# Optimization experiments

Hardware: AMD Instinct MI355X
Metric: run time of the kernel (lower is better)

The kernel has to match this reference:

```python
import jax, jax.numpy as jnp
import numpy as np
from jax import lax

B, T, C = 32, 512, 128
K = 3                      # top_k periods
MIN_P, MAX_P = 8, 64       # period search band
P_MAX = MAX_P              # grid width
CYC_MAX = (T + MIN_P - 1) // MIN_P
KW = 9                     # cyc-axis depthwise kernel
GN_G = 32                  # _best_gn_groups(128)
EPS_GN = 1e-5
EPS_ORTH = 1e-6
EPS_W = 1e-8


def setup_inputs() -> dict:
    key = jax.random.key(0)
    ks = jax.random.split(key, 4)
    return {
        "x": jax.random.normal(ks[0], (B, T, C), jnp.float32),
        "W_dw": jax.random.normal(ks[1], (C, 1, KW), jnp.float32) * 0.1,
        "W_pw": jax.random.normal(ks[2], (C, C), jnp.float32) * (1.0 / np.sqrt(C)),
        "gn_weight": jnp.ones((C,), jnp.float32),
        "gn_bias": jnp.zeros((C,), jnp.float32),
        "W_gate": jax.random.normal(ks[3], (C, C), jnp.float32) * (1.0 / np.sqrt(C)),
        "gamma": jnp.full((C,), 1e-3, jnp.float32),
    }


def _autocorr_topk(x):
    # x: [B,T,C] -> period idx [B,K], softmax weights [B,K]
    Xf = jnp.fft.rfft(x, axis=1)
    Pm = (Xf * jnp.conj(Xf)).real.mean(-1)          # [B, T//2+1]
    r = jnp.fft.irfft(Pm, n=T, axis=1)              # [B, T] autocorrelation
    lag = jnp.arange(T)
    valid = (lag >= MIN_P) & (lag <= MAX_P)
    very_neg = jnp.finfo(x.dtype).min / 8
    rm = jnp.where(valid[None, :], r, very_neg)
    vals, idx = lax.top_k(rm, K)
    w = jax.nn.softmax(vals, axis=1)
    return idx, w


def _fold(s, p):
    # s: [N,T,C], p: [N] int periods -> Z [N,C,CYC_MAX,P_MAX], mask, unfold index maps
    N = s.shape[0]
    p = jnp.maximum(p, 1)
    tpad = ((T + p - 1) // p) * p                   # [N]
    cyc = jnp.arange(CYC_MAX)[None, :, None]
    pos = jnp.arange(P_MAX)[None, None, :]
    time = cyc * p[:, None, None] + pos             # [N,CYC_MAX,P_MAX]
    valid = (pos < p[:, None, None]) & (time < tpad[:, None, None])
    # right-side reflect padding indices
    m = 2 * (T - 1)
    rr = time % m
    src_idx = jnp.where(rr < T, rr, m - rr)
    src = jnp.take_along_axis(s, src_idx.reshape(N, -1)[:, :, None], axis=1)
    src = src.reshape(N, CYC_MAX, P_MAX, C) * valid[..., None].astype(s.dtype)
    Z = jnp.transpose(src, (0, 3, 1, 2))            # [N,C,CYC_MAX,P_MAX]
    mask2d = valid[:, None].astype(s.dtype)         # [N,1,CYC_MAX,P_MAX]
    t = jnp.arange(T)[None, :]
    cyc_T = jnp.clip(t // p[:, None], 0, CYC_MAX - 1)
    pos_T = jnp.clip(t % p[:, None], 0, P_MAX - 1)
    return Z, mask2d, cyc_T, pos_T


def _cyc_conv(Z, mask2d, W_dw, W_pw, gn_w, gn_b, W_gate, gamma):
    # CycAxisConv1d: mean over period axis, depthwise+pointwise conv along cyc,
    # GroupNorm, GELU, SE-gate, LayerScale residual broadcast back to 2D.
    N, _, L, _ = Z.shape
    u = Z.mean(-1)                                  # [N,C,L]
    h = lax.conv_general_dilated(u, W_dw, (1,), [(KW // 2, KW // 2)],
                                 dimension_numbers=('NCH', 'OIH', 'NCH'),
                                 feature_group_count=C)
    h = jnp.einsum('oc,ncl->nol', W_pw, h)
    hg = h.reshape(N, GN_G, C // GN_G, L)
    mean = hg.mean((2, 3), keepdims=True)
    var = hg.var((2, 3), keepdims=True)
    hg = (hg - mean) * lax.rsqrt(var + EPS_GN)
    h = hg.reshape(N, C, L) * gn_w[None, :, None] + gn_b[None, :, None]
    h = jax.nn.gelu(h, approximate=False)
    gate = jax.nn.sigmoid(jnp.einsum('oc,nc->no', W_gate, u.mean(-1)))
    h = h * gate[:, :, None]
    x2d = h[..., None] * gamma[None, :, None, None] * mask2d
    return Z + x2d


def _unfold(Z, cyc_T, pos_T):
    N = Z.shape[0]
    Zf = Z.reshape(N, C, CYC_MAX * P_MAX)
    sp = jnp.clip(cyc_T * P_MAX + pos_T, 0, CYC_MAX * P_MAX - 1)  # [N,T]
    y = jnp.take_along_axis(Zf, sp[:, None, :], axis=2)           # [N,C,T]
    return jnp.transpose(y, (0, 2, 1))                            # [N,T,C]


def reference(x, W_dw, W_pw, gn_weight, gn_bias, W_gate, gamma):
    idx, w = _autocorr_topk(x)                      # [B,K], [B,K]
    p_flat = idx.reshape(-1)                        # [B*K]
    s = jnp.repeat(x, K, axis=0)                    # [B*K,T,C]
    Z, mask2d, cyc_T, pos_T = _fold(s, p_flat)
    Z = _cyc_conv(Z, mask2d, W_dw, W_pw, gn_weight, gn_bias, W_gate, gamma)
    y = _unfold(Z, cyc_T, pos_T).reshape(B, K, T, C)
    periodic = jnp.einsum('bk,bktc->btc', w, y)
    # period confidence Gamma from weight entropy
    H = -(w * jnp.log(w + EPS_W)).sum(1)
    Gamma = jnp.clip(1.0 - H / (jnp.log(float(K) + EPS_W) + EPS_W), 0.0, 1.0)
    # orthogonal residual of local part against periodic part
    local = x - periodic
    num = (local * periodic).sum(1, keepdims=True)
    den = (periodic * periodic).sum(1, keepdims=True) + EPS_ORTH
    local_orth = local - num / den * periodic
    g = Gamma[:, None, None]
    return g * (periodic + local_orth) + (1.0 - g) * x
```

## Files before the change

### kernel.cpp

```cpp
#include <hip/hip_runtime.h>
#include <math.h>

static constexpr int Bn   = 32;
static constexpr int Tn   = 512;
static constexpr int Cn   = 128;
static constexpr int NLAG = 57;
static constexpr int CYC  = 64;

__device__ __forceinline__ int topk_p(const float* __restrict__ rb,
                                      int tid, int kk) {
  float v  = (tid < NLAG) ? rb[tid] : -INFINITY;
  int  idx = tid;
  int  lag = 8;
#pragma unroll
  for (int k = 0; k < 3; ++k) {
    if (k > kk) break;
    float bv = v; int bi = idx;
#pragma unroll
    for (int m = 32; m > 0; m >>= 1) {
      const float ov = __shfl_xor(bv, m, 64);
      const int   oi = __shfl_xor(bi, m, 64);
      if (ov > bv || (ov == bv && oi < bi)) { bv = ov; bi = oi; }
    }
    lag = bi + 8;
    if (idx == bi) v = -INFINITY;
  }
  return lag;
}

__global__ __launch_bounds__(256) void k_autocorr(const float* __restrict__ x,
    float* __restrict__ r_ws) {
  const int w   = (blockIdx.x & 7) * 32 + (blockIdx.x >> 3);
  const int b   = w >> 3;
  const int grp = w & 7;
  const int L0  = 8 + grp * 8;
  const int tid = threadIdx.x;
  const float4* X4 = (const float4*)(x + (size_t)b * Tn * Cn);

  float acc[8];
#pragma unroll
  for (int i = 0; i < 8; ++i) acc[i] = 0.f;

  for (int it = 0; it < 8; ++it) {
    const int id = it * 256 + tid;
    const int c4 = id & 31;
    const int t0 = (id >> 5) * 8;
    float4 A[8];
#pragma unroll
    for (int j = 0; j < 8; ++j) A[j] = X4[(t0 + j) * 32 + c4];
    float4 R[16];
#pragma unroll
    for (int j = 0; j < 16; ++j) R[j] = X4[((t0 + L0 + j) & 511) * 32 + c4];
#pragma unroll
    for (int g = 0; g < 8; ++g) {
#pragma unroll
      for (int j = 0; j < 8; ++j) {
        const float4 a = A[j];
        const float4 r = R[g + j];
        acc[g] += a.x * r.x + a.y * r.y + a.z * r.z + a.w * r.w;
      }
    }
  }

  __shared__ float lds_r[4][8];
  const int lane = tid & 63, wave = tid >> 6;
#pragma unroll
  for (int g = 0; g < 8; ++g) {
    float v = acc[g];
#pragma unroll
    for (int m = 32; m > 0; m >>= 1) v += __shfl_xor(v, m, 64);
    if (lane == 0) lds_r[wave][g] = v;
  }
  __syncthreads();
  if (tid < 8) {
    const int li = grp * 8 + tid;
    if (li < NLAG) {
      r_ws[b * NLAG + li] =
          (lds_r[0][tid] + lds_r[1][tid] + lds_r[2][tid] + lds_r[3][tid]) * (1.0f / Cn);
    }
  }
}

__global__ __launch_bounds__(128) void k_fold_u(const float* __restrict__ x,
    const float* __restrict__ r_ws, float* __restrict__ u) {
  const int bid = blockIdx.x;
  const int w = (bid & 7) * 768 + (bid >> 3);
  const int n = w >> 6, l = w & 63;
  const int b = n / 3, kk = n % 3;
  const int tid = threadIdx.x;

  __shared__ int p_sh;
  if (tid < 64) {
    const int lag = topk_p(r_ws + b * NLAG, tid, kk);
    if (tid == 0) p_sh = lag;
  }
  __syncthreads();
  const int p    = p_sh;
  const int ncyc = (Tn + p - 1) / p;

  float acc = 0.f;
  if (l < ncyc) {
    const float* xb = x + (size_t)b * Tn * Cn;
    const int base = l * p;
    for (int j = 0; j < p; ++j) {
      const int time = base + j;
      const int src  = time < Tn ? time : (2 * (Tn - 1) - time);
      acc += xb[src * Cn + tid];
    }
  }
  u[((size_t)n * CYC + l) * Cn + tid] = acc * (1.0f / 64.0f);
}

__global__ __launch_bounds__(256) void k_conv(
    const float* __restrict__ u, const float* __restrict__ Wdw,
    const float* __restrict__ Wpw, const float* __restrict__ gnw,
    const float* __restrict__ gnb, const float* __restrict__ Wgate,
    float* __restrict__ hh) {
  const int bid = blockIdx.x;
  const int w = (bid & 7) * 96 + (bid >> 3);
  const int n = w >> 3, og = w & 7;
  const int tid  = threadIdx.x;
  const int l    = tid & 63;
  const int wq   = __builtin_amdgcn_readfirstlane(tid >> 6);

  __shared__ float smem[8320];
  __shared__ float ubar_s[Cn];

  {
    const float4* u4 = (const float4*)(u + (size_t)n * CYC * Cn);
#pragma unroll
    for (int i = 0; i < 8; ++i) {
      const int idx4 = i * 256 + tid;
      const float4 v = u4[idx4];
      const int ll = idx4 >> 5;
      const int cc = (idx4 & 31) << 2;
      float* d = smem + ll * 129 + cc;
      d[0] = v.x; d[1] = v.y; d[2] = v.z; d[3] = v.w;
    }
  }
  __syncthreads();

  if (tid < Cn) {
    float s = 0.f;
    for (int ll = 0; ll < CYC; ++ll) s += smem[ll * 129 + tid];
    ubar_s[tid] = s * (1.0f / CYC);
  }

  float hreg[32];
  {
    const int c0 = wq * 32;
#pragma unroll
    for (int i = 0; i < 32; ++i) {
      const int c = c0 + i;
      float s = 0.f;
#pragma unroll
      for (int k = 0; k < 9; ++k) {
        const int ll = l + k - 4;
        if (ll >= 0 && ll < CYC) s += smem[ll * 129 + c] * Wdw[c * 9 + k];
      }
      hreg[i] = s;
    }
  }
  __syncthreads();

  float gi[4];
  {
    const int ol   = l & 3;
    const int part = l >> 2;
    const int o    = og * 16 + wq * 4 + ol;
    float z = 0.f;
    const float* wg = Wgate + (size_t)o * Cn + part * 8;
    const float* ub = ubar_s + part * 8;
#pragma unroll
    for (int cc = 0; cc < 8; ++cc) z += wg[cc] * ub[cc];
    z += __shfl_xor(z, 4, 64);
    z += __shfl_xor(z, 8, 64);
    z += __shfl_xor(z, 16, 64);
    z += __shfl_xor(z, 32, 64);
    const float sig = 1.0f / (1.0f + expf(-z));
#pragma unroll
    for (int i = 0; i < 4; ++i) gi[i] = __shfl(sig, i, 64);
  }

  {
    const int c0 = wq * 32;
#pragma unroll
    for (int i = 0; i < 32; ++i) smem[(c0 + i) * 65 + l] = hreg[i];
  }
  __syncthreads();

  const int o4 = og * 16 + wq * 4;
  float acc[4];
#pragma unroll
  for (int i = 0; i < 4; ++i) acc[i] = 0.f;
  const float* wb = Wpw + (size_t)o4 * Cn;
  for (int c = 0; c < Cn; ++c) {
    const float hv = smem[c * 65 + l];
#pragma unroll
    for (int i = 0; i < 4; ++i) acc[i] = fmaf(wb[i * Cn + c], hv, acc[i]);
  }

  float s1 = acc[0] + acc[1] + acc[2] + acc[3];
  float s2 = acc[0]*acc[0] + acc[1]*acc[1] + acc[2]*acc[2] + acc[3]*acc[3];
#pragma unroll
  for (int m = 32; m > 0; m >>= 1) {
    s1 += __shfl_xor(s1, m, 64);
    s2 += __shfl_xor(s2, m, 64);
  }
  const float mean = s1 * (1.0f / 256.0f);
  const float var  = s2 * (1.0f / 256.0f) - mean * mean;
  const float rstd = rsqrtf(var + 1e-5f);

  float4 res;
  float* rp = (float*)&res;
#pragma unroll
  for (int i = 0; i < 4; ++i) {
    const int o = o4 + i;
    float h = (acc[i] - mean) * rstd;
    h = h * gnw[o] + gnb[o];
    h = 0.5f * h * (1.0f + erff(h * 0.70710678118654752440f));
    rp[i] = h * gi[i];
  }
  *(float4*)(hh + (size_t)n * CYC * Cn + (size_t)l * Cn + o4) = res;
}

__global__ __launch_bounds__(256) void k_dot_out(
    const float* __restrict__ x, const float* __restrict__ hh,
    const float* __restrict__ r_ws, const float* __restrict__ gamma,
    float* __restrict__ out) {
  const int bid = blockIdx.x;
  const int w = (bid & 7) * 32 + (bid >> 3);
  const int b = w >> 3, cg = w & 7;
  const int tid = threadIdx.x;
  const int c_l = tid & 15;
  const int tg  = tid >> 4;
  const int c   = cg * 16 + c_l;

  __shared__ float P_s[Tn * 16];
  __shared__ unsigned short cyc_s[Tn][3];
  __shared__ float params[4];
  __shared__ int   pp[3];
  __shared__ float red[2][4][16];
  __shared__ float sc_s[16];

  if (tid < 64) {
    const float* rb = r_ws + b * NLAG;
    float v  = (tid < NLAG) ? rb[tid] : -INFINITY;
    int  idx = tid;
    float vals[3]; int lags[3];
#pragma unroll
    for (int k = 0; k < 3; ++k) {
      float bv = v; int bi = idx;
#pragma unroll
      for (int m = 32; m > 0; m >>= 1) {
        const float ov = __shfl_xor(bv, m, 64);
        const int   oi = __shfl_xor(bi, m, 64);
        if (ov > bv || (ov == bv && oi < bi)) { bv = ov; bi = oi; }
      }
      vals[k] = bv; lags[k] = bi + 8;
      if (idx == bi) v = -INFINITY;
    }
    if (tid == 0) {
      const float m  = vals[0];
      const float e0 = expf(vals[0] - m), e1 = expf(vals[1] - m), e2 = expf(vals[2] - m);
      const float s  = e0 + e1 + e2;
      const float w0 = e0 / s, w1 = e1 / s, w2 = e2 / s;
      pp[0] = lags[0]; pp[1] = lags[1]; pp[2] = lags[2];
      params[0] = w0; params[1] = w1; params[2] = w2;
      const float H  = -(w0 * logf(w0 + 1e-8f) + w1 * logf(w1 + 1e-8f) + w2 * logf(w2 + 1e-8f));
      const float lg = logf(3.0f + 1e-8f) + 1e-8f;
      params[3] = fminf(fmaxf(1.0f - H / lg, 0.0f), 1.0f);
    }
  }
  __syncthreads();
  const int p0 = pp[0], p1 = pp[1], p2 = pp[2];
  const float w0 = params[0], w1 = params[1], w2 = params[2];
  const float g  = params[3];
  const float sw = w0 + w1 + w2;

  for (int t = tid; t < Tn; t += 256) {
    cyc_s[t][0] = (unsigned short)(t / p0);
    cyc_s[t][1] = (unsigned short)(t / p1);
    cyc_s[t][2] = (unsigned short)(t / p2);
  }
  __syncthreads();

  const float gam = gamma[c];
  const float* xb = x + (size_t)b * Tn * Cn;
  const float* h0 = hh + (size_t)(b * 3 + 0) * CYC * Cn + c;
  const float* h1 = hh + (size_t)(b * 3 + 1) * CYC * Cn + c;
  const float* h2 = hh + (size_t)(b * 3 + 2) * CYC * Cn + c;

  float na = 0.f, da = 0.f;
#pragma unroll 4
  for (int tt = 0; tt < 32; ++tt) {
    const int t = tt * 16 + tg;
    const float xv = xb[t * Cn + c];
    const float dv = gam * (w0 * h0[cyc_s[t][0] * Cn] +
                            w1 * h1[cyc_s[t][1] * Cn] +
                            w2 * h2[cyc_s[t][2] * Cn]);
    const float P = sw * xv + dv;
    P_s[t * 16 + c_l] = P;
    na += (xv - P) * P;
    da += P * P;
  }
  na += __shfl_xor(na, 16, 64); da += __shfl_xor(da, 16, 64);
  na += __shfl_xor(na, 32, 64); da += __shfl_xor(da, 32, 64);
  const int wv_ = tid >> 6;
  if ((tid & 63) < 16) { red[0][wv_][c_l] = na; red[1][wv_][c_l] = da; }
  __syncthreads();
  if (tid < 16) {
    const float num = red[0][0][tid] + red[0][1][tid] + red[0][2][tid] + red[0][3][tid];
    const float den = red[1][0][tid] + red[1][1][tid] + red[1][2][tid] + red[1][3][tid] + 1e-6f;
    sc_s[tid] = g * (num / den);
  }
  __syncthreads();
  const float sc = sc_s[c_l];

  float* ob = out + (size_t)b * Tn * Cn;
#pragma unroll 4
  for (int tt = 0; tt < 32; ++tt) {
    const int t = tt * 16 + tg;
    const float xv = xb[t * Cn + c];
    ob[t * Cn + c] = xv - sc * P_s[t * 16 + c_l];
  }
}

extern "C" void kernel_launch(void* const* d_in, const int* in_sizes, int n_in,
                              void* d_out, int out_size, void* d_ws, size_t ws_size,
                              hipStream_t stream) {
  const float* x     = (const float*)d_in[0];
  const float* Wdw   = (const float*)d_in[1];
  const float* Wpw   = (const float*)d_in[2];
  const float* gnw   = (const float*)d_in[3];
  const float* gnb   = (const float*)d_in[4];
  const float* Wgate = (const float*)d_in[5];
  const float* gamma = (const float*)d_in[6];
  float* out = (float*)d_out;

  char* ws = (char*)d_ws;
  float* r_ws = (float*)ws;
  float* u    = (float*)(ws + 8192);
  float* hh   = (float*)(ws + 8192 + 3145728);

  k_autocorr<<<Bn * 8, 256, 0, stream>>>(x, r_ws);
  k_fold_u<<<6144, 128, 0, stream>>>(x, r_ws, u);
  k_conv<<<768, 256, 0, stream>>>(u, Wdw, Wpw, gnw, gnb, Wgate, hh);
  k_dot_out<<<256, 256, 0, stream>>>(x, hh, r_ws, gamma, out);
}
```

Measured before the change: 138.9 us.

## Fuse four kernels into one cooperative persistent kernel with grid syncs

Replaces the four-kernel chain (autocorr, fold, conv, output) with a single cooperative kernel of 512 blocks that runs each stage in turn, separated by grid.sync(). Work is remapped per stage: autocorr uses 16 groups of 4 lags per batch, fold runs 12 units per block, and conv runs 1 or 2 units per block. The aim is to remove kernel launch gaps and tail effects between stages. In exchange it adds grid-wide barrier cost and uneven work per block in the conv and output stages. If the cooperative launch fails, it falls back to the old four launches.

```diff
diff --git a/kernel.cpp b/kernel.cpp
--- a/kernel.cpp
+++ b/kernel.cpp
@@ -1,5 +1,8 @@
 #include <hip/hip_runtime.h>
+#include <hip/hip_cooperative_groups.h>
 #include <math.h>
+
+namespace cg = cooperative_groups;
 
 static constexpr int Bn   = 32;
 static constexpr int Tn   = 512;
@@ -8,9 +11,9 @@
 static constexpr int CYC  = 64;
 
 __device__ __forceinline__ int topk_p(const float* __restrict__ rb,
-                                      int tid, int kk) {
-  float v  = (tid < NLAG) ? rb[tid] : -INFINITY;
-  int  idx = tid;
+                                      int lane, int kk) {
+  float v  = (lane < NLAG) ? rb[lane] : -INFINITY;
+  int  idx = lane;
   int  lag = 8;
 #pragma unroll
   for (int k = 0; k < 3; ++k) {
@@ -26,6 +29,320 @@
     if (idx == bi) v = -INFINITY;
   }
   return lag;
+}
+
+__device__ __forceinline__ void conv_unit(
+    int n, int og, int tid,
+    const float* __restrict__ u, const float* __restrict__ Wdw,
+    const float* __restrict__ Wpw, const float* __restrict__ gnw,
+    const float* __restrict__ gnb, const float* __restrict__ Wgate,
+    float* __restrict__ hh, float* smem, float* ubar_s) {
+  const int l  = tid & 63;
+  const int wq = __builtin_amdgcn_readfirstlane(tid >> 6);
+
+  __syncthreads();
+
+  {
+    const float4* u4 = (const float4*)(u + (size_t)n * CYC * Cn);
+#pragma unroll
+    for (int i = 0; i < 8; ++i) {
+      const int idx4 = i * 256 + tid;
+      const float4 v = u4[idx4];
+      const int ll = idx4 >> 5;
+      const int cc = (idx4 & 31) << 2;
+      float* d = smem + ll * 129 + cc;
+      d[0] = v.x; d[1] = v.y; d[2] = v.z; d[3] = v.w;
+    }
+  }
+  __syncthreads();
+
+  if (tid < Cn) {
+    float s = 0.f;
+    for (int ll = 0; ll < CYC; ++ll) s += smem[ll * 129 + tid];
+    ubar_s[tid] = s * (1.0f / CYC);
+  }
+
+  float hreg[32];
+  {
+    const int c0 = wq * 32;
+#pragma unroll
+    for (int i = 0; i < 32; ++i) {
+      const int c = c0 + i;
+      float s = 0.f;
+#pragma unroll
+      for (int k = 0; k < 9; ++k) {
+        const int ll = l + k - 4;
+        if (ll >= 0 && ll < CYC) s += smem[ll * 129 + c] * Wdw[c * 9 + k];
+      }
+      hreg[i] = s;
+    }
+  }
+  __syncthreads();
+
+  float gi[4];
+  {
+    const int ol   = l & 3;
+    const int part = l >> 2;
+    const int o    = og * 16 + wq * 4 + ol;
+    float z = 0.f;
+    const float* wg = Wgate + (size_t)o * Cn + part * 8;
+    const float* ub = ubar_s + part * 8;
+#pragma unroll
+    for (int cc = 0; cc < 8; ++cc) z += wg[cc] * ub[cc];
+    z += __shfl_xor(z, 4, 64);
+    z += __shfl_xor(z, 8, 64);
+    z += __shfl_xor(z, 16, 64);
+    z += __shfl_xor(z, 32, 64);
+    const float sig = 1.0f / (1.0f + expf(-z));
+#pragma unroll
+    for (int i = 0; i < 4; ++i) gi[i] = __shfl(sig, i, 64);
+  }
+
+  {
+    const int c0 = wq * 32;
+#pragma unroll
+    for (int i = 0; i < 32; ++i) smem[(c0 + i) * 65 + l] = hreg[i];
+  }
+  __syncthreads();
+
+  const int o4 = og * 16 + wq * 4;
+  float acc[4];
+#pragma unroll
+  for (int i = 0; i < 4; ++i) acc[i] = 0.f;
+  const float* wb = Wpw + (size_t)o4 * Cn;
+  for (int c = 0; c < Cn; ++c) {
+    const float hv = smem[c * 65 + l];
+#pragma unroll
+    for (int i = 0; i < 4; ++i) acc[i] = fmaf(wb[i * Cn + c], hv, acc[i]);
+  }
+
+  float s1 = acc[0] + acc[1] + acc[2] + acc[3];
+  float s2 = acc[0]*acc[0] + acc[1]*acc[1] + acc[2]*acc[2] + acc[3]*acc[3];
+#pragma unroll
+  for (int m = 32; m > 0; m >>= 1) {
+    s1 += __shfl_xor(s1, m, 64);
+    s2 += __shfl_xor(s2, m, 64);
+  }
+  const float mean = s1 * (1.0f / 256.0f);
+  const float var  = s2 * (1.0f / 256.0f) - mean * mean;
+  const float rstd = rsqrtf(var + 1e-5f);
+
+  float4 res;
+  float* rp = (float*)&res;
+#pragma unroll
+  for (int i = 0; i < 4; ++i) {
+    const int o = o4 + i;
+    float h = (acc[i] - mean) * rstd;
+    h = h * gnw[o] + gnb[o];
+    h = 0.5f * h * (1.0f + erff(h * 0.70710678118654752440f));
+    rp[i] = h * gi[i];
+  }
+  *(float4*)(hh + (size_t)n * CYC * Cn + (size_t)l * Cn + o4) = res;
+}
+
+__global__ __launch_bounds__(256, 2) void mega(
+    const float* __restrict__ x, const float* __restrict__ Wdw,
+    const float* __restrict__ Wpw, const float* __restrict__ gnw,
+    const float* __restrict__ gnb, const float* __restrict__ Wgate,
+    const float* __restrict__ gamma, float* __restrict__ r_ws,
+    float* __restrict__ u, float* __restrict__ hh, float* __restrict__ out) {
+  cg::grid_group grid = cg::this_grid();
+  const int bid = blockIdx.x;
+  const int ws  = (bid & 7) * 64 + (bid >> 3);
+  const int xcd = ws >> 6;
+  const int tid = threadIdx.x;
+
+  __shared__ float smem[8320];
+  __shared__ float ubar_s[Cn];
+  __shared__ unsigned short cyc_s[Tn][3];
+  __shared__ float ldsr[4][4];
+  __shared__ int   pslot[12];
+  __shared__ float red_s[2][4][16];
+  __shared__ float sc_s[16];
+  __shared__ float par_s[4];
+  __shared__ int   pp_s[3];
+
+  {
+    const int b   = ws >> 4;
+    const int grp = ws & 15;
+    const int L0  = 8 + grp * 4;
+    const float4* X4 = (const float4*)(x + (size_t)b * Tn * Cn);
+
+    float acc[4];
+#pragma unroll
+    for (int i = 0; i < 4; ++i) acc[i] = 0.f;
+
+    for (int it = 0; it < 8; ++it) {
+      const int id = it * 256 + tid;
+      const int c4 = id & 31;
+      const int t0 = (id >> 5) * 8;
+      float4 A[8];
+#pragma unroll
+      for (int j = 0; j < 8; ++j) A[j] = X4[(t0 + j) * 32 + c4];
+      float4 R[11];
+#pragma unroll
+      for (int j = 0; j < 11; ++j) R[j] = X4[((t0 + L0 + j) & 511) * 32 + c4];
+#pragma unroll
+      for (int g = 0; g < 4; ++g) {
+#pragma unroll
+        for (int j = 0; j < 8; ++j) {
+          const float4 a = A[j];
+          const float4 r = R[g + j];
+          acc[g] += a.x * r.x + a.y * r.y + a.z * r.z + a.w * r.w;
+        }
+      }
+    }
+
+    const int lane = tid & 63, wv = tid >> 6;
+#pragma unroll
+    for (int g = 0; g < 4; ++g) {
+      float v = acc[g];
+#pragma unroll
+      for (int m = 32; m > 0; m >>= 1) v += __shfl_xor(v, m, 64);
+      if (lane == 0) ldsr[wv][g] = v;
+    }
+    __syncthreads();
+    if (tid < 4) {
+      const int li = grp * 4 + tid;
+      if (li < NLAG) {
+        r_ws[b * NLAG + li] =
+            (ldsr[0][tid] + ldsr[1][tid] + ldsr[2][tid] + ldsr[3][tid]) * (1.0f / Cn);
+      }
+    }
+  }
+  grid.sync();
+
+  {
+    for (int it2 = 0; it2 < 6; ++it2) {
+      const int sub  = tid >> 7;
+      const int unit = ws * 12 + it2 * 2 + sub;
+      const int n = unit >> 6, l = unit & 63;
+      const int b = n / 3, kk = n % 3;
+      if ((tid & 64) == 0) {
+        const int lag = topk_p(r_ws + b * NLAG, tid & 63, kk);
+        if ((tid & 63) == 0) pslot[it2 * 2 + sub] = lag;
+      }
+      __syncthreads();
+      const int p    = pslot[it2 * 2 + sub];
+      const int ncyc = (Tn + p - 1) / p;
+      const int c    = tid & 127;
+      float acc = 0.f;
+      if (l < ncyc) {
+        const float* xb = x + (size_t)b * Tn * Cn;
+        const int base = l * p;
+        for (int j = 0; j < p; ++j) {
+          const int time = base + j;
+          const int src  = time < Tn ? time : (2 * (Tn - 1) - time);
+          acc += xb[src * Cn + c];
+        }
+      }
+      u[((size_t)n * CYC + l) * Cn + c] = acc * (1.0f / 64.0f);
+    }
+  }
+  grid.sync();
+
+  {
+    const int j0 = ws & 63;
+    conv_unit(12 * xcd + (j0 >> 3), j0 & 7, tid,
+              u, Wdw, Wpw, gnw, gnb, Wgate, hh, smem, ubar_s);
+    if (bid < 256) {
+      const int j1 = 64 + (ws & 31);
+      conv_unit(12 * xcd + (j1 >> 3), j1 & 7, tid,
+                u, Wdw, Wpw, gnw, gnb, Wgate, hh, smem, ubar_s);
+    }
+  }
+  grid.sync();
+
+  if (bid < 256) {
+    const int unit = xcd * 32 + (ws & 31);
+    const int b = unit >> 3, cgp = unit & 7;
+    const int c_l = tid & 15;
+    const int tg  = tid >> 4;
+    const int c   = cgp * 16 + c_l;
+    float* P_s = smem;
+
+    if (tid < 64) {
+      const float* rb = r_ws + b * NLAG;
+      float v  = (tid < NLAG) ? rb[tid] : -INFINITY;
+      int  idx = tid;
+      float vals[3]; int lags[3];
+#pragma unroll
+      for (int k = 0; k < 3; ++k) {
+        float bv = v; int bi = idx;
+#pragma unroll
+        for (int m = 32; m > 0; m >>= 1) {
+          const float ov = __shfl_xor(bv, m, 64);
+          const int   oi = __shfl_xor(bi, m, 64);
+          if (ov > bv || (ov == bv && oi < bi)) { bv = ov; bi = oi; }
+        }
+        vals[k] = bv; lags[k] = bi + 8;
+        if (idx == bi) v = -INFINITY;
+      }
+      if (tid == 0) {
+        const float m  = vals[0];
+        const float e0 = expf(vals[0] - m), e1 = expf(vals[1] - m), e2 = expf(vals[2] - m);
+        const float s  = e0 + e1 + e2;
+        const float w0 = e0 / s, w1 = e1 / s, w2 = e2 / s;
+        pp_s[0] = lags[0]; pp_s[1] = lags[1]; pp_s[2] = lags[2];
+        par_s[0] = w0; par_s[1] = w1; par_s[2] = w2;
+        const float H  = -(w0 * logf(w0 + 1e-8f) + w1 * logf(w1 + 1e-8f) + w2 * logf(w2 + 1e-8f));
+        const float lg = logf(3.0f + 1e-8f) + 1e-8f;
+        par_s[3] = fminf(fmaxf(1.0f - H / lg, 0.0f), 1.0f);
+      }
+    }
+    __syncthreads();
+    const int p0 = pp_s[0], p1 = pp_s[1], p2 = pp_s[2];
+    const float w0 = par_s[0], w1 = par_s[1], w2 = par_s[2];
+    const float g  = par_s[3];
+    const float sw = w0 + w1 + w2;
+
+    for (int t = tid; t < Tn; t += 256) {
+      cyc_s[t][0] = (unsigned short)(t / p0);
+      cyc_s[t][1] = (unsigned short)(t / p1);
+      cyc_s[t][2] = (unsigned short)(t / p2);
+    }
+    __syncthreads();
+
+    const float gam = gamma[c];
+    const float* xb = x + (size_t)b * Tn * Cn;
+    const float* h0 = hh + (size_t)(b * 3 + 0) * CYC * Cn + c;
+    const float* h1 = hh + (size_t)(b * 3 + 1) * CYC * Cn + c;
+    const float* h2 = hh + (size_t)(b * 3 + 2) * CYC * Cn + c;
+
+    float na = 0.f, da = 0.f;
+#pragma unroll 4
+    for (int tt = 0; tt < 32; ++tt) {
+      const int t = tt * 16 + tg;
+      const float xv = xb[t * Cn + c];
+      const float dv = gam * (w0 * h0[cyc_s[t][0] * Cn] +
+                              w1 * h1[cyc_s[t][1] * Cn] +
+                              w2 * h2[cyc_s[t][2] * Cn]);
+      const float P = sw * xv + dv;
+      P_s[t * 16 + c_l] = P;
+      na += (xv - P) * P;
+      da += P * P;
+    }
+    na += __shfl_xor(na, 16, 64); da += __shfl_xor(da, 16, 64);
+    na += __shfl_xor(na, 32, 64); da += __shfl_xor(da, 32, 64);
+    const int wv_ = tid >> 6;
+    if ((tid & 63) < 16) { red_s[0][wv_][c_l] = na; red_s[1][wv_][c_l] = da; }
+    __syncthreads();
+    if (tid < 16) {
+      const float num = red_s[0][0][tid] + red_s[0][1][tid] + red_s[0][2][tid] + red_s[0][3][tid];
+      const float den = red_s[1][0][tid] + red_s[1][1][tid] + red_s[1][2][tid] + red_s[1][3][tid] + 1e-6f;
+      sc_s[tid] = g * (num / den);
+    }
+    __syncthreads();
+    const float sc = sc_s[c_l];
+
+    float* ob = out + (size_t)b * Tn * Cn;
+#pragma unroll 4
+    for (int tt = 0; tt < 32; ++tt) {
+      const int t = tt * 16 + tg;
+      const float xv = xb[t * Cn + c];
+      ob[t * Cn + c] = xv - sc * P_s[t * 16 + c_l];
+    }
+  }
 }
 
 __global__ __launch_bounds__(256) void k_autocorr(const float* __restrict__ x,
@@ -40,7 +357,6 @@
   float acc[8];
 #pragma unroll
   for (int i = 0; i < 8; ++i) acc[i] = 0.f;
-
   for (int it = 0; it < 8; ++it) {
     const int id = it * 256 + tid;
     const int c4 = id & 31;
@@ -61,7 +377,6 @@
       }
     }
   }
-
   __shared__ float lds_r[4][8];
   const int lane = tid & 63, wave = tid >> 6;
 #pragma unroll
@@ -74,10 +389,9 @@
   __syncthreads();
   if (tid < 8) {
     const int li = grp * 8 + tid;
-    if (li < NLAG) {
+    if (li < NLAG)
       r_ws[b * NLAG + li] =
           (lds_r[0][tid] + lds_r[1][tid] + lds_r[2][tid] + lds_r[3][tid]) * (1.0f / Cn);
-    }
   }
 }
 
@@ -88,16 +402,14 @@
   const int n = w >> 6, l = w & 63;
   const int b = n / 3, kk = n % 3;
   const int tid = threadIdx.x;
-
   __shared__ int p_sh;
   if (tid < 64) {
     const int lag = topk_p(r_ws + b * NLAG, tid, kk);
     if (tid == 0) p_sh = lag;
   }
   __syncthreads();
-  const int p    = p_sh;
+  const int p = p_sh;
   const int ncyc = (Tn + p - 1) / p;
-
   float acc = 0.f;
   if (l < ncyc) {
     const float* xb = x + (size_t)b * Tn * Cn;
@@ -119,109 +431,9 @@
   const int bid = blockIdx.x;
   const int w = (bid & 7) * 96 + (bid >> 3);
   const int n = w >> 3, og = w & 7;
-  const int tid  = threadIdx.x;
-  const int l    = tid & 63;
-  const int wq   = __builtin_amdgcn_readfirstlane(tid >> 6);
-
   __shared__ float smem[8320];
   __shared__ float ubar_s[Cn];
-
-  {
-    const float4* u4 = (const float4*)(u + (size_t)n * CYC * Cn);
-#pragma unroll
-    for (int i = 0; i < 8; ++i) {
-      const int idx4 = i * 256 + tid;
-      const float4 v = u4[idx4];
-      const int ll = idx4 >> 5;
-      const int cc = (idx4 & 31) << 2;
-      float* d = smem + ll * 129 + cc;
-      d[0] = v.x; d[1] = v.y; d[2] = v.z; d[3] = v.w;
-    }
-  }
-  __syncthreads();
-
-  if (tid < Cn) {
-    float s = 0.f;
-    for (int ll = 0; ll < CYC; ++ll) s += smem[ll * 129 + tid];
-    ubar_s[tid] = s * (1.0f / CYC);
-  }
-
-  float hreg[32];
-  {
-    const int c0 = wq * 32;
-#pragma unroll
-    for (int i = 0; i < 32; ++i) {
-      const int c = c0 + i;
-      float s = 0.f;
-#pragma unroll
-      for (int k = 0; k < 9; ++k) {
-        const int ll = l + k - 4;
-        if (ll >= 0 && ll < CYC) s += smem[ll * 129 + c] * Wdw[c * 9 + k];
-      }
-      hreg[i] = s;
-    }
-  }
-  __syncthreads();
-
-  float gi[4];
-  {
-    const int ol   = l & 3;
-    const int part = l >> 2;
-    const int o    = og * 16 + wq * 4 + ol;
-    float z = 0.f;
-    const float* wg = Wgate + (size_t)o * Cn + part * 8;
-    const float* ub = ubar_s + part * 8;
-#pragma unroll
-    for (int cc = 0; cc < 8; ++cc) z += wg[cc] * ub[cc];
-    z += __shfl_xor(z, 4, 64);
-    z += __shfl_xor(z, 8, 64);
-    z += __shfl_xor(z, 16, 64);
-    z += __shfl_xor(z, 32, 64);
-    const float sig = 1.0f / (1.0f + expf(-z));
-#pragma unroll
-    for (int i = 0; i < 4; ++i) gi[i] = __shfl(sig, i, 64);
-  }
-
-  {
-    const int c0 = wq * 32;
-#pragma unroll
-    for (int i = 0; i < 32; ++i) smem[(c0 + i) * 65 + l] = hreg[i];
-  }
-  __syncthreads();
-
-  const int o4 = og * 16 + wq * 4;
-  float acc[4];
-#pragma unroll
-  for (int i = 0; i < 4; ++i) acc[i] = 0.f;
-  const float* wb = Wpw + (size_t)o4 * Cn;
-  for (int c = 0; c < Cn; ++c) {
-    const float hv = smem[c * 65 + l];
-#pragma unroll
-    for (int i = 0; i < 4; ++i) acc[i] = fmaf(wb[i * Cn + c], hv, acc[i]);
-  }
-
-  float s1 = acc[0] + acc[1] + acc[2] + acc[3];
-  float s2 = acc[0]*acc[0] + acc[1]*acc[1] + acc[2]*acc[2] + acc[3]*acc[3];
-#pragma unroll
-  for (int m = 32; m > 0; m >>= 1) {
-    s1 += __shfl_xor(s1, m, 64);
-    s2 += __shfl_xor(s2, m, 64);
-  }
-  const float mean = s1 * (1.0f / 256.0f);
-  const float var  = s2 * (1.0f / 256.0f) - mean * mean;
-  const float rstd = rsqrtf(var + 1e-5f);
-
-  float4 res;
-  float* rp = (float*)&res;
-#pragma unroll
-  for (int i = 0; i < 4; ++i) {
-    const int o = o4 + i;
-    float h = (acc[i] - mean) * rstd;
-    h = h * gnw[o] + gnb[o];
-    h = 0.5f * h * (1.0f + erff(h * 0.70710678118654752440f));
-    rp[i] = h * gi[i];
-  }
-  *(float4*)(hh + (size_t)n * CYC * Cn + (size_t)l * Cn + o4) = res;
+  conv_unit(n, og, threadIdx.x, u, Wdw, Wpw, gnw, gnb, Wgate, hh, smem, ubar_s);
 }
 
 __global__ __launch_bounds__(256) void k_dot_out(
@@ -343,8 +555,18 @@
   float* u    = (float*)(ws + 8192);
   float* hh   = (float*)(ws + 8192 + 3145728);
 
-  k_autocorr<<<Bn * 8, 256, 0, stream>>>(x, r_ws);
-  k_fold_u<<<6144, 128, 0, stream>>>(x, r_ws, u);
-  k_conv<<<768, 256, 0, stream>>>(u, Wdw, Wpw, gnw, gnb, Wgate, hh);
-  k_dot_out<<<256, 256, 0, stream>>>(x, hh, r_ws, gamma, out);
-}
+  void* args[] = {
+    (void*)&x, (void*)&Wdw, (void*)&Wpw, (void*)&gnw, (void*)&gnb,
+    (void*)&Wgate, (void*)&gamma, (void*)&r_ws, (void*)&u, (void*)&hh,
+    (void*)&out
+  };
+  hipError_t e = hipLaunchCooperativeKernel((const void*)mega, dim3(512),
+                                            dim3(256), args, 0, stream);
+  if (e != hipSuccess) {
+    (void)hipGetLastError();
+    k_autocorr<<<Bn * 8, 256, 0, stream>>>(x, r_ws);
+    k_fold_u<<<6144, 128, 0, stream>>>(x, r_ws, u);
+    k_conv<<<768, 256, 0, stream>>>(u, Wdw, Wpw, gnw, gnb, Wgate, hh);
+    k_dot_out<<<256, 256, 0, stream>>>(x, hh, r_ws, gamma, out);
+  }
+}
```

Result: slower. 385.7 us (+177.7%).
